# Performance work log

Hardware: AMD Instinct MI355X
Metric: run time of the kernel (lower is better)

## Reference

```python
import jax, jax.numpy as jnp
import numpy as np

N_NODES = 50000
N_EDGES = 800000
IN_F, OUT_F, N_HEADS = 128, 64, 4
NEG_SLOPE = 0.2
EPS = 1e-12


def setup_inputs() -> dict:
    key = jax.random.key(0)
    ks = jax.random.split(key, 6)
    x = jax.random.normal(ks[0], (N_NODES, IN_F), dtype=jnp.float32)
    edge_index = jax.random.randint(ks[1], (2, N_EDGES), 0, N_NODES, dtype=jnp.int32)
    # xavier-uniform-like scaled params
    W = jax.random.normal(ks[2], (IN_F, OUT_F), dtype=jnp.float32) * (2.0 / (IN_F + OUT_F)) ** 0.5
    a_l = jax.random.normal(ks[3], (OUT_F, N_HEADS), dtype=jnp.float32) * (2.0 / (OUT_F + N_HEADS)) ** 0.5
    a_r = jax.random.normal(ks[4], (OUT_F, N_HEADS), dtype=jnp.float32) * (2.0 / (OUT_F + N_HEADS)) ** 0.5
    b = jnp.zeros((OUT_F,), dtype=jnp.float32)
    return {"x": x, "edge_index": edge_index, "W": W, "a_l": a_l, "a_r": a_r, "b": b}


def reference(x, edge_index, W, a_l, a_r, b):
    # GATConv forward (eval mode: attn dropout is identity).
    # Dense NxNxH scatter + L1 normalize in the original == per-row edge softmax
    # over exp(leaky_relu(el[row]+er[col])); honor edge sparsity directly.
    n = x.shape[0]
    h = x @ W                      # [N, D] node representations
    el = h @ a_l                   # [N, H] left (dst/row) scores
    er = h @ a_r                   # [N, H] right (src/col) scores
    row, col = edge_index[0], edge_index[1]
    e = el[row] + er[col]          # [E, H]
    e = jnp.where(e > 0, e, NEG_SLOPE * e)   # leaky_relu(0.2)
    e = jnp.exp(e)
    denom = jax.ops.segment_sum(e, row, num_segments=n)        # [N, H]
    attn = e / jnp.maximum(denom[row], EPS)                    # [E, H] L1-normalized per row
    msg = attn[:, :, None] * h[col][:, None, :]                # [E, H, D]
    out = jax.ops.segment_sum(msg, row, num_segments=n)        # [N, H, D]
    out = out + b                                              # bias broadcast over heads
    return out.reshape(n, -1)                                  # [N, H*D]
```

## Files before the change

kernel.cpp:

```cpp
#include <hip/hip_runtime.h>

#define N_NODES 50000
#define N_EDGES 800000
#define IN_F    128
#define OUT_F   64
#define N_HEADS 4
#define NEG_SLOPE 0.2f
#define EPS 1e-12f

#define NODE_BLOCKS 782
#define NB    391
#define CHUNK 4096
#define NCH   196
#define S2N   (NB * NCH)
#define S2B   75

typedef __attribute__((ext_vector_type(8))) short bf16x8;
typedef __attribute__((ext_vector_type(4))) float f32x4;
typedef __attribute__((ext_vector_type(4))) unsigned int u32x4;

__device__ __forceinline__ unsigned short f2bf(float f) {
    unsigned int u = __float_as_uint(f);
    u += 0x7FFFu + ((u >> 16) & 1u);
    return (unsigned short)(u >> 16);
}
__device__ __forceinline__ float bf_lo(unsigned u) { return __uint_as_float(u << 16); }
__device__ __forceinline__ float bf_hi(unsigned u) { return __uint_as_float(u & 0xFFFF0000u); }

__global__ __launch_bounds__(256) void k_hist_gemm(
    const float* __restrict__ x, const float* __restrict__ W,
    const float* __restrict__ a_l, const float* __restrict__ a_r,
    const int* __restrict__ row, int* __restrict__ histG,
    unsigned short* __restrict__ h_bf,
    float* __restrict__ el, float* __restrict__ er)
{
    __shared__ int hist[NB];
    __shared__ unsigned short xs[64 * 128];
    __shared__ unsigned short wsh[64 * 128];
    const int tid = threadIdx.x;

    if (blockIdx.x < NCH) {
        const int ch = blockIdx.x;
        for (int i = tid; i < NB; i += 256) hist[i] = 0;
        __syncthreads();
        const int e0 = ch * CHUNK + tid * 16;
        #pragma unroll
        for (int q = 0; q < 4; ++q) {
            const int e = e0 + q * 4;
            if (e + 3 < N_EDGES) {
                int4 a = *(const int4*)(row + e);
                atomicAdd(&hist[a.x >> 7], 1); atomicAdd(&hist[a.y >> 7], 1);
                atomicAdd(&hist[a.z >> 7], 1); atomicAdd(&hist[a.w >> 7], 1);
            } else {
                #pragma unroll
                for (int j = 0; j < 4; ++j)
                    if (e + j < N_EDGES) atomicAdd(&hist[row[e + j] >> 7], 1);
            }
        }
        __syncthreads();
        for (int i = tid; i < NB; i += 256) histG[i * NCH + ch] = hist[i];
        return;
    }

    const int node0 = (blockIdx.x - NCH) * 64;

    {
        const int c  = tid & 63;
        const int kq = tid >> 6;
        #pragma unroll
        for (int kb = 0; kb < 32; kb += 8) {
            unsigned pk[4];
            #pragma unroll
            for (int i = 0; i < 4; ++i) {
                const int k = kq * 32 + kb + 2 * i;
                const float v0 = W[k * OUT_F + c];
                const float v1 = W[(k + 1) * OUT_F + c];
                pk[i] = (unsigned)f2bf(v0) | ((unsigned)f2bf(v1) << 16);
            }
            const int cb = (kq * 32 + kb) * 2;
            *(uint4*)((char*)wsh + c * 256 + (cb ^ ((c & 7) << 4))) =
                make_uint4(pk[0], pk[1], pk[2], pk[3]);
        }
    }
    {
        const int r = tid >> 2;
        const int c0 = (tid & 3) * 32;
        const int node = node0 + r;
        unsigned int pk[16];
        if (node < N_NODES) {
            const float* src = x + (size_t)node * IN_F + c0;
            #pragma unroll
            for (int i = 0; i < 8; ++i) {
                float4 v = *(const float4*)(src + 4 * i);
                pk[2 * i + 0] = (unsigned)f2bf(v.x) | ((unsigned)f2bf(v.y) << 16);
                pk[2 * i + 1] = (unsigned)f2bf(v.z) | ((unsigned)f2bf(v.w) << 16);
            }
        } else {
            #pragma unroll
            for (int i = 0; i < 16; ++i) pk[i] = 0;
        }
        #pragma unroll
        for (int q = 0; q < 4; ++q) {
            int cb = c0 * 2 + q * 16;
            *(uint4*)((char*)xs + r * 256 + (cb ^ ((r & 7) << 4))) =
                make_uint4(pk[4 * q], pk[4 * q + 1], pk[4 * q + 2], pk[4 * q + 3]);
        }
    }
    __syncthreads();

    const int w  = tid >> 6, l = tid & 63;
    const int lr = l & 15, lg = l >> 4;
    const int arow = w * 16 + lr;

    bf16x8 afr[4];
    #pragma unroll
    for (int t = 0; t < 4; ++t) {
        int cb = t * 64 + lg * 16;
        afr[t] = *(const bf16x8*)((char*)xs + arow * 256 + (cb ^ ((arow & 7) << 4)));
    }

    const f32x4 zero = {0.f, 0.f, 0.f, 0.f};
    f32x4 acc[4] = {zero, zero, zero, zero};
    #pragma unroll
    for (int nt = 0; nt < 4; ++nt) {
        const int brow = nt * 16 + lr;
        #pragma unroll
        for (int t = 0; t < 4; ++t) {
            int cb = t * 64 + lg * 16;
            bf16x8 bfr = *(const bf16x8*)((char*)wsh + brow * 256 + (cb ^ ((brow & 7) << 4)));
            acc[nt] = __builtin_amdgcn_mfma_f32_16x16x32_bf16(afr[t], bfr, acc[nt], 0, 0, 0);
        }
    }

    #pragma unroll
    for (int r = 0; r < 4; ++r) {
        const int node = node0 + w * 16 + lg * 4 + r;
        if (node < N_NODES) {
            #pragma unroll
            for (int nt = 0; nt < 4; ++nt)
                h_bf[(size_t)node * OUT_F + nt * 16 + lr] = f2bf(acc[nt][r]);
        }
    }

    float4 al4[4], ar4[4];
    #pragma unroll
    for (int nt = 0; nt < 4; ++nt) {
        al4[nt] = *(const float4*)(a_l + (size_t)(nt * 16 + lr) * N_HEADS);
        ar4[nt] = *(const float4*)(a_r + (size_t)(nt * 16 + lr) * N_HEADS);
    }
    #pragma unroll
    for (int r = 0; r < 4; ++r) {
        float4 pl = make_float4(0.f, 0.f, 0.f, 0.f);
        float4 pr = make_float4(0.f, 0.f, 0.f, 0.f);
        #pragma unroll
        for (int nt = 0; nt < 4; ++nt) {
            const float v = acc[nt][r];
            pl.x += v * al4[nt].x; pl.y += v * al4[nt].y;
            pl.z += v * al4[nt].z; pl.w += v * al4[nt].w;
            pr.x += v * ar4[nt].x; pr.y += v * ar4[nt].y;
            pr.z += v * ar4[nt].z; pr.w += v * ar4[nt].w;
        }
        #pragma unroll
        for (int off = 1; off < 16; off <<= 1) {
            pl.x += __shfl_xor(pl.x, off); pl.y += __shfl_xor(pl.y, off);
            pl.z += __shfl_xor(pl.z, off); pl.w += __shfl_xor(pl.w, off);
            pr.x += __shfl_xor(pr.x, off); pr.y += __shfl_xor(pr.y, off);
            pr.z += __shfl_xor(pr.w = pr.w, off) * 0.f + __shfl_xor(pr.z, off);
            pr.w += __shfl_xor(pr.w, off);
        }
        const int node = node0 + w * 16 + lg * 4 + r;
        if (lr == 0 && node < N_NODES) {
            *(float4*)(el + (size_t)node * N_HEADS) = pl;
            *(float4*)(er + (size_t)node * N_HEADS) = pr;
        }
    }
}

__global__ __launch_bounds__(256) void k_scan2_local(
    const int* __restrict__ histG, int* __restrict__ scanHist,
    int* __restrict__ blocksum)
{
    __shared__ int wsum[4];
    const int t = threadIdx.x;
    const int base = blockIdx.x * 1024 + t * 4;

    int4 d = make_int4(0, 0, 0, 0);
    if (base + 3 < S2N) d = *(const int4*)(histG + base);
    else {
        if (base + 0 < S2N) d.x = histG[base + 0];
        if (base + 1 < S2N) d.y = histG[base + 1];
        if (base + 2 < S2N) d.z = histG[base + 2];
        if (base + 3 < S2N) d.w = histG[base + 3];
    }
    const int tsum = d.x + d.y + d.z + d.w;

    const int lane = t & 63, wave = t >> 6;
    int inc = tsum;
    #pragma unroll
    for (int off = 1; off < 64; off <<= 1) {
        int v = __shfl_up(inc, off);
        if (lane >= off) inc += v;
    }
    if (lane == 63) wsum[wave] = inc;
    __syncthreads();

    int woff = 0;
    #pragma unroll
    for (int w = 0; w < 4; ++w) woff += (w < wave) ? wsum[w] : 0;

    const int ex = woff + inc - tsum;
    int4 o;
    o.x = ex; o.y = ex + d.x; o.z = o.y + d.y; o.w = o.z + d.z;
    if (base + 3 < S2N) *(int4*)(scanHist + base) = o;
    else {
        if (base + 0 < S2N) scanHist[base + 0] = o.x;
        if (base + 1 < S2N) scanHist[base + 1] = o.y;
        if (base + 2 < S2N) scanHist[base + 2] = o.z;
        if (base + 3 < S2N) scanHist[base + 3] = o.w;
    }
    if (t == 0) blocksum[blockIdx.x] = wsum[0] + wsum[1] + wsum[2] + wsum[3];
}

__global__ __launch_bounds__(256) void k_scatter(
    const int* __restrict__ row, const int* __restrict__ col,
    const int* __restrict__ scanHist, const int* __restrict__ blocksum,
    unsigned* __restrict__ ebuf)
{
    __shared__ int off[NB];
    __shared__ int bsum[S2B];
    const int ch = blockIdx.x;
    const int t = threadIdx.x;
    if (t < S2B) bsum[t] = blocksum[t];
    __syncthreads();
    if (t == 0) {
        int s = 0;
        for (int i = 0; i < S2B; ++i) { int v = bsum[i]; bsum[i] = s; s += v; }
    }
    __syncthreads();
    for (int i = t; i < NB; i += 256) {
        const int idx = i * NCH + ch;
        off[i] = scanHist[idx] + bsum[idx >> 10];
    }
    __syncthreads();
    const int e0 = ch * CHUNK;
    #pragma unroll
    for (int k = 0; k < 16; ++k) {
        const int e = e0 + t + k * 256;
        if (e < N_EDGES) {
            const int r = row[e], c = col[e];
            const int pos = atomicAdd(&off[r >> 7], 1);
            ebuf[pos] = ((unsigned)(r & 127) << 17) | (unsigned)c;
        }
    }
}

__global__ __launch_bounds__(256) void k_bucket(
    const unsigned* __restrict__ ebuf, const int* __restrict__ scanHist,
    const int* __restrict__ blocksum,
    const float* __restrict__ el, const float* __restrict__ er,
    int* __restrict__ rowptr, uint4* __restrict__ edata)
{
    __shared__ float4 elv[128];
    __shared__ int cnt[128];
    __shared__ int wsum2[2];
    __shared__ int bsum[S2B];
    const int b = blockIdx.x;
    const int t = threadIdx.x;
    const int node0 = b << 7;

    if (t < S2B) bsum[t] = blocksum[t];
    __syncthreads();
    if (t == 0) {
        int s = 0;
        for (int i = 0; i < S2B; ++i) { int v = bsum[i]; bsum[i] = s; s += v; }
    }
    __syncthreads();

    const int i0 = b * NCH;
    const int base = scanHist[i0] + bsum[i0 >> 10];
    int end;
    if (b < NB - 1) {
        const int i1 = (b + 1) * NCH;
        end = scanHist[i1] + bsum[i1 >> 10];
    } else end = N_EDGES;

    if (t < 128) {
        const int node = node0 + t;
        elv[t] = (node < N_NODES) ? *(const float4*)(el + node * 4)
                                  : make_float4(0.f, 0.f, 0.f, 0.f);
        cnt[t] = 0;
    }
    __syncthreads();
    for (int i = base + t; i < end; i += 256)
        atomicAdd(&cnt[ebuf[i] >> 17], 1);
    __syncthreads();

    int inc = 0, val = 0;
    const int lane = t & 63, wave = t >> 6;
    if (t < 128) {
        val = cnt[t];
        inc = val;
        #pragma unroll
        for (int off = 1; off < 64; off <<= 1) {
            int v = __shfl_up(inc, off);
            if (lane >= off) inc += v;
        }
        if (lane == 63) wsum2[wave] = inc;
    }
    __syncthreads();
    int excl = 0;
    if (t < 128) {
        const int woff = (wave == 1) ? wsum2[0] : 0;
        excl = base + woff + inc - val;
        const int node = node0 + t;
        if (node < N_NODES) rowptr[node] = excl;
    }
    if (b == NB - 1 && t == 0) rowptr[N_NODES] = N_EDGES;
    __syncthreads();
    if (t < 128) cnt[t] = excl;
    __syncthreads();

    for (int i = base + t; i < end; i += 256) {
        const unsigned p = ebuf[i];
        const int r = p >> 17;
        const int c = (int)(p & 0x1FFFFu);
        const int pos = atomicAdd(&cnt[r], 1);
        const float4 e4 = elv[r];
        const float4 r4 = *(const float4*)(er + ((unsigned)c << 2));
        float s0 = e4.x + r4.x, s1 = e4.y + r4.y;
        float s2 = e4.z + r4.z, s3 = e4.w + r4.w;
        s0 = s0 > 0.f ? s0 : NEG_SLOPE * s0;
        s1 = s1 > 0.f ? s1 : NEG_SLOPE * s1;
        s2 = s2 > 0.f ? s2 : NEG_SLOPE * s2;
        s3 = s3 > 0.f ? s3 : NEG_SLOPE * s3;
        const unsigned w01 = (unsigned)f2bf(__expf(s0)) | ((unsigned)f2bf(__expf(s1)) << 16);
        const unsigned w23 = (unsigned)f2bf(__expf(s2)) | ((unsigned)f2bf(__expf(s3)) << 16);
        edata[pos] = make_uint4((unsigned)c, w01, w23, 0u);
    }
}

__global__ __launch_bounds__(256) void k_gather(
    const int* __restrict__ rowptr, const u32x4* __restrict__ edata,
    const unsigned short* __restrict__ h_bf, const float* __restrict__ b,
    float* __restrict__ out)
{
    int n = blockIdx.x * 4 + (threadIdx.x >> 6);
    if (n >= N_NODES) return;
    const int lane = threadIdx.x & 63;
    const int g    = lane >> 4;
    const int fq   = lane & 15;

    const int s0 = rowptr[n], s1 = rowptr[n + 1];
    const int nit = (s1 - s0 + 7) >> 3;

    float acc[4][4];
    #pragma unroll
    for (int hd = 0; hd < 4; ++hd)
        #pragma unroll
        for (int f = 0; f < 4; ++f) acc[hd][f] = 0.f;
    float den[4] = {0.f, 0.f, 0.f, 0.f};

    if (nit > 0) {
#define LOADE(ii, E0, E1)                                       \
        {                                                       \
            const int j0 = s0 + (ii) * 8 + 2 * g;               \
            const int j1 = j0 + 1;                              \
            E0 = __builtin_nontemporal_load(&edata[j0 < s1 ? j0 : s1 - 1]); \
            E1 = __builtin_nontemporal_load(&edata[j1 < s1 ? j1 : s1 - 1]); \
            if (j0 >= s1) { E0.y = 0u; E0.z = 0u; }             \
            if (j1 >= s1) { E1.y = 0u; E1.z = 0u; }             \
        }
#define LOADH(E, H)                                                              \
        H = *(const uint2*)(h_bf + (((E.x & 0xFFFFu) << 6) + ((unsigned)fq << 2)));
#define COMP1(E, H)                                                              \
        {                                                                        \
            const float w0 = bf_lo(E.y), w1 = bf_hi(E.y);                        \
            const float w2 = bf_lo(E.z), w3 = bf_hi(E.z);                        \
            const float f0 = bf_lo(H.x), f1 = bf_hi(H.x);                        \
            const float f2 = bf_lo(H.y), f3 = bf_hi(H.y);                        \
            den[0] += w0; den[1] += w1; den[2] += w2; den[3] += w3;              \
            acc[0][0] += w0 * f0; acc[0][1] += w0 * f1;                          \
            acc[0][2] += w0 * f2; acc[0][3] += w0 * f3;                          \
            acc[1][0] += w1 * f0; acc[1][1] += w1 * f1;                          \
            acc[1][2] += w1 * f2; acc[1][3] += w1 * f3;                          \
            acc[2][0] += w2 * f0; acc[2][1] += w2 * f1;                          \
            acc[2][2] += w2 * f2; acc[2][3] += w2 * f3;                          \
            acc[3][0] += w3 * f0; acc[3][1] += w3 * f1;                          \
            acc[3][2] += w3 * f2; acc[3][3] += w3 * f3;                          \
        }

        u32x4 a0, a1, b0, b1;
        uint2 ha0, ha1, hb0, hb1;
        LOADE(0, a0, a1);
        LOADH(a0, ha0); LOADH(a1, ha1);

        for (int it = 0; it < nit; ++it) {
            LOADE(it + 1, b0, b1);
            LOADH(b0, hb0); LOADH(b1, hb1);
            COMP1(a0, ha0);
            COMP1(a1, ha1);
            a0 = b0; a1 = b1; ha0 = hb0; ha1 = hb1;
        }
#undef LOADE
#undef LOADH
#undef COMP1
    }

    #pragma unroll
    for (int hd = 0; hd < 4; ++hd) {
        float v = den[hd];
        v += __shfl_xor(v, 16); v += __shfl_xor(v, 32);
        den[hd] = v;
        #pragma unroll
        for (int f = 0; f < 4; ++f) {
            float u = acc[hd][f];
            u += __shfl_xor(u, 16); u += __shfl_xor(u, 32);
            acc[hd][f] = u;
        }
    }

    const float dg = g == 0 ? den[0] : g == 1 ? den[1] : g == 2 ? den[2] : den[3];
    const float inv = 1.f / fmaxf(dg, EPS);
    f32x4 o;
    o.x = (g == 0 ? acc[0][0] : g == 1 ? acc[1][0] : g == 2 ? acc[2][0] : acc[3][0]);
    o.y = (g == 0 ? acc[0][1] : g == 1 ? acc[1][1] : g == 2 ? acc[2][1] : acc[3][1]);
    o.z = (g == 0 ? acc[0][2] : g == 1 ? acc[1][2] : g == 2 ? acc[2][2] : acc[3][2]);
    o.w = (g == 0 ? acc[0][3] : g == 1 ? acc[1][3] : g == 2 ? acc[2][3] : acc[3][3]);

    const float4 bias = *(const float4*)(b + fq * 4);
    o.x = o.x * inv + bias.x;
    o.y = o.y * inv + bias.y;
    o.z = o.z * inv + bias.z;
    o.w = o.w * inv + bias.w;
    __builtin_nontemporal_store(o,
        (f32x4*)(out + (size_t)n * (N_HEADS * OUT_F) + g * 64 + fq * 4));
}

extern "C" void kernel_launch(void* const* d_in, const int* in_sizes, int n_in,
                              void* d_out, int out_size, void* d_ws, size_t ws_size,
                              hipStream_t stream)
{
    const float* x   = (const float*)d_in[0];
    const int*   ei  = (const int*)d_in[1];
    const float* W   = (const float*)d_in[2];
    const float* a_l = (const float*)d_in[3];
    const float* a_r = (const float*)d_in[4];
    const float* b   = (const float*)d_in[5];
    float* out = (float*)d_out;

    char* ws = (char*)d_ws;
    unsigned short* h_bf = (unsigned short*)(ws);
    float*    el       = (float*)   (ws +  6400000);
    float*    er       = (float*)   (ws +  7200000);
    int*      histG    = (int*)     (ws +  8000000);
    int*      scanHist = (int*)     (ws +  8306544);
    int*      blocksum = (int*)     (ws +  8613088);
    unsigned* ebuf     = (unsigned*)(ws +  8614112);
    int*      rowptr   = (int*)     (ws + 11814112);
    uint4*    edata    = (uint4*)   (ws + 12014128);

    const int* row = ei;
    const int* col = ei + N_EDGES;

    k_hist_gemm  <<<NCH + NODE_BLOCKS, 256, 0, stream>>>(
                     x, W, a_l, a_r, row, histG, h_bf, el, er);
    k_scan2_local<<<S2B, 256, 0, stream>>>(histG, scanHist, blocksum);
    k_scatter    <<<NCH, 256, 0, stream>>>(row, col, scanHist, blocksum, ebuf);
    k_bucket     <<<NB, 256, 0, stream>>>(ebuf, scanHist, blocksum, el, er, rowptr, edata);
    k_gather     <<<N_NODES / 4, 256, 0, stream>>>(rowptr, (const u32x4*)edata, h_bf, b, out);
}
```

Measured before the change: 81.20 us.

## Fuse scan, scatter and bucket kernels into one kernel with grid barriers

Merges the three middle kernels (histogram scan, edge scatter, per-bucket CSR build) into one persistent kernel of 391 blocks. The stages are separated by software grid barriers built on atomic counters, which the first kernel resets. This removes two kernel launches and their inter-kernel gaps. It relies on all 391 blocks being co-resident, which launch_bounds(256,2) is meant to help with, or the barrier deadlocks. The gather kernel also drops its nontemporal loads of the edge data in favour of plain loads.

Measured after the change: 155.5 us. 91.6% more time.

```diff
diff --git a/kernel.cpp b/kernel.cpp
--- a/kernel.cpp
+++ b/kernel.cpp
@@ -17,7 +17,6 @@
 
 typedef __attribute__((ext_vector_type(8))) short bf16x8;
 typedef __attribute__((ext_vector_type(4))) float f32x4;
-typedef __attribute__((ext_vector_type(4))) unsigned int u32x4;
 
 __device__ __forceinline__ unsigned short f2bf(float f) {
     unsigned int u = __float_as_uint(f);
@@ -26,13 +25,26 @@
 }
 __device__ __forceinline__ float bf_lo(unsigned u) { return __uint_as_float(u << 16); }
 __device__ __forceinline__ float bf_hi(unsigned u) { return __uint_as_float(u & 0xFFFF0000u); }
+
+__device__ __forceinline__ void gbar(int* ctr, int nblk) {
+    __syncthreads();
+    if (threadIdx.x == 0) {
+        __threadfence();
+        atomicAdd(ctr, 1);
+        while (__hip_atomic_load(ctr, __ATOMIC_RELAXED, __HIP_MEMORY_SCOPE_AGENT) < nblk)
+            __builtin_amdgcn_s_sleep(1);
+        __threadfence();
+    }
+    __syncthreads();
+}
 
 __global__ __launch_bounds__(256) void k_hist_gemm(
     const float* __restrict__ x, const float* __restrict__ W,
     const float* __restrict__ a_l, const float* __restrict__ a_r,
     const int* __restrict__ row, int* __restrict__ histG,
     unsigned short* __restrict__ h_bf,
-    float* __restrict__ el, float* __restrict__ er)
+    float* __restrict__ el, float* __restrict__ er,
+    int* __restrict__ sync_ctr)
 {
     __shared__ int hist[NB];
     __shared__ unsigned short xs[64 * 128];
@@ -41,6 +53,7 @@
 
     if (blockIdx.x < NCH) {
         const int ch = blockIdx.x;
+        if (ch == 0 && tid < 8) sync_ctr[tid] = 0;
         for (int i = tid; i < NB; i += 256) hist[i] = 0;
         __syncthreads();
         const int e0 = ch * CHUNK + tid * 16;
@@ -165,8 +178,7 @@
             pl.x += __shfl_xor(pl.x, off); pl.y += __shfl_xor(pl.y, off);
             pl.z += __shfl_xor(pl.z, off); pl.w += __shfl_xor(pl.w, off);
             pr.x += __shfl_xor(pr.x, off); pr.y += __shfl_xor(pr.y, off);
-            pr.z += __shfl_xor(pr.w = pr.w, off) * 0.f + __shfl_xor(pr.z, off);
-            pr.w += __shfl_xor(pr.w, off);
+            pr.z += __shfl_xor(pr.z, off); pr.w += __shfl_xor(pr.w, off);
         }
         const int node = node0 + w * 16 + lg * 4 + r;
         if (lr == 0 && node < N_NODES) {
@@ -176,60 +188,60 @@
     }
 }
 
-__global__ __launch_bounds__(256) void k_scan2_local(
+__global__ __launch_bounds__(256, 2) void k_build(
+    const int* __restrict__ row, const int* __restrict__ col,
     const int* __restrict__ histG, int* __restrict__ scanHist,
-    int* __restrict__ blocksum)
-{
-    __shared__ int wsum[4];
-    const int t = threadIdx.x;
-    const int base = blockIdx.x * 1024 + t * 4;
-
-    int4 d = make_int4(0, 0, 0, 0);
-    if (base + 3 < S2N) d = *(const int4*)(histG + base);
-    else {
-        if (base + 0 < S2N) d.x = histG[base + 0];
-        if (base + 1 < S2N) d.y = histG[base + 1];
-        if (base + 2 < S2N) d.z = histG[base + 2];
-        if (base + 3 < S2N) d.w = histG[base + 3];
-    }
-    const int tsum = d.x + d.y + d.z + d.w;
-
-    const int lane = t & 63, wave = t >> 6;
-    int inc = tsum;
-    #pragma unroll
-    for (int off = 1; off < 64; off <<= 1) {
-        int v = __shfl_up(inc, off);
-        if (lane >= off) inc += v;
-    }
-    if (lane == 63) wsum[wave] = inc;
-    __syncthreads();
-
-    int woff = 0;
-    #pragma unroll
-    for (int w = 0; w < 4; ++w) woff += (w < wave) ? wsum[w] : 0;
-
-    const int ex = woff + inc - tsum;
-    int4 o;
-    o.x = ex; o.y = ex + d.x; o.z = o.y + d.y; o.w = o.z + d.z;
-    if (base + 3 < S2N) *(int4*)(scanHist + base) = o;
-    else {
-        if (base + 0 < S2N) scanHist[base + 0] = o.x;
-        if (base + 1 < S2N) scanHist[base + 1] = o.y;
-        if (base + 2 < S2N) scanHist[base + 2] = o.z;
-        if (base + 3 < S2N) scanHist[base + 3] = o.w;
-    }
-    if (t == 0) blocksum[blockIdx.x] = wsum[0] + wsum[1] + wsum[2] + wsum[3];
-}
-
-__global__ __launch_bounds__(256) void k_scatter(
-    const int* __restrict__ row, const int* __restrict__ col,
-    const int* __restrict__ scanHist, const int* __restrict__ blocksum,
-    unsigned* __restrict__ ebuf)
+    int* __restrict__ blocksum,
+    const float* __restrict__ el, const float* __restrict__ er,
+    unsigned* __restrict__ ebuf, int* __restrict__ rowptr,
+    uint4* __restrict__ edata, int* __restrict__ sync_ctr)
 {
     __shared__ int off[NB];
     __shared__ int bsum[S2B];
-    const int ch = blockIdx.x;
+    __shared__ float4 elv[128];
+    __shared__ int cnt[128];
+    __shared__ int wsum4[4];
+    const int blk = blockIdx.x;
     const int t = threadIdx.x;
+
+    if (blk < S2B) {
+        const int base = blk * 1024 + t * 4;
+        int4 d = make_int4(0, 0, 0, 0);
+        if (base + 3 < S2N) d = *(const int4*)(histG + base);
+        else {
+            if (base + 0 < S2N) d.x = histG[base + 0];
+            if (base + 1 < S2N) d.y = histG[base + 1];
+            if (base + 2 < S2N) d.z = histG[base + 2];
+            if (base + 3 < S2N) d.w = histG[base + 3];
+        }
+        const int tsum = d.x + d.y + d.z + d.w;
+        const int lane = t & 63, wave = t >> 6;
+        int inc = tsum;
+        #pragma unroll
+        for (int off2 = 1; off2 < 64; off2 <<= 1) {
+            int v = __shfl_up(inc, off2);
+            if (lane >= off2) inc += v;
+        }
+        if (lane == 63) wsum4[wave] = inc;
+        __syncthreads();
+        int woff = 0;
+        #pragma unroll
+        for (int w = 0; w < 4; ++w) woff += (w < wave) ? wsum4[w] : 0;
+        const int ex = woff + inc - tsum;
+        int4 o;
+        o.x = ex; o.y = ex + d.x; o.z = o.y + d.y; o.w = o.z + d.z;
+        if (base + 3 < S2N) *(int4*)(scanHist + base) = o;
+        else {
+            if (base + 0 < S2N) scanHist[base + 0] = o.x;
+            if (base + 1 < S2N) scanHist[base + 1] = o.y;
+            if (base + 2 < S2N) scanHist[base + 2] = o.z;
+            if (base + 3 < S2N) scanHist[base + 3] = o.w;
+        }
+        if (t == 0) blocksum[blk] = wsum4[0] + wsum4[1] + wsum4[2] + wsum4[3];
+    }
+
+    gbar(&sync_ctr[0], NB);
+
     if (t < S2B) bsum[t] = blocksum[t];
     __syncthreads();
     if (t == 0) {
@@ -237,110 +249,97 @@
         for (int i = 0; i < S2B; ++i) { int v = bsum[i]; bsum[i] = s; s += v; }
     }
     __syncthreads();
-    for (int i = t; i < NB; i += 256) {
-        const int idx = i * NCH + ch;
-        off[i] = scanHist[idx] + bsum[idx >> 10];
-    }
-    __syncthreads();
-    const int e0 = ch * CHUNK;
-    #pragma unroll
-    for (int k = 0; k < 16; ++k) {
-        const int e = e0 + t + k * 256;
-        if (e < N_EDGES) {
-            const int r = row[e], c = col[e];
-            const int pos = atomicAdd(&off[r >> 7], 1);
-            ebuf[pos] = ((unsigned)(r & 127) << 17) | (unsigned)c;
-        }
-    }
-}
-
-__global__ __launch_bounds__(256) void k_bucket(
-    const unsigned* __restrict__ ebuf, const int* __restrict__ scanHist,
-    const int* __restrict__ blocksum,
-    const float* __restrict__ el, const float* __restrict__ er,
-    int* __restrict__ rowptr, uint4* __restrict__ edata)
-{
-    __shared__ float4 elv[128];
-    __shared__ int cnt[128];
-    __shared__ int wsum2[2];
-    __shared__ int bsum[S2B];
-    const int b = blockIdx.x;
-    const int t = threadIdx.x;
-    const int node0 = b << 7;
-
-    if (t < S2B) bsum[t] = blocksum[t];
-    __syncthreads();
-    if (t == 0) {
-        int s = 0;
-        for (int i = 0; i < S2B; ++i) { int v = bsum[i]; bsum[i] = s; s += v; }
-    }
-    __syncthreads();
-
-    const int i0 = b * NCH;
-    const int base = scanHist[i0] + bsum[i0 >> 10];
-    int end;
-    if (b < NB - 1) {
-        const int i1 = (b + 1) * NCH;
-        end = scanHist[i1] + bsum[i1 >> 10];
-    } else end = N_EDGES;
-
-    if (t < 128) {
-        const int node = node0 + t;
-        elv[t] = (node < N_NODES) ? *(const float4*)(el + node * 4)
-                                  : make_float4(0.f, 0.f, 0.f, 0.f);
-        cnt[t] = 0;
-    }
-    __syncthreads();
-    for (int i = base + t; i < end; i += 256)
-        atomicAdd(&cnt[ebuf[i] >> 17], 1);
-    __syncthreads();
-
-    int inc = 0, val = 0;
-    const int lane = t & 63, wave = t >> 6;
-    if (t < 128) {
-        val = cnt[t];
-        inc = val;
-        #pragma unroll
-        for (int off = 1; off < 64; off <<= 1) {
-            int v = __shfl_up(inc, off);
-            if (lane >= off) inc += v;
-        }
-        if (lane == 63) wsum2[wave] = inc;
-    }
-    __syncthreads();
-    int excl = 0;
-    if (t < 128) {
-        const int woff = (wave == 1) ? wsum2[0] : 0;
-        excl = base + woff + inc - val;
-        const int node = node0 + t;
-        if (node < N_NODES) rowptr[node] = excl;
-    }
-    if (b == NB - 1 && t == 0) rowptr[N_NODES] = N_EDGES;
-    __syncthreads();
-    if (t < 128) cnt[t] = excl;
-    __syncthreads();
-
-    for (int i = base + t; i < end; i += 256) {
-        const unsigned p = ebuf[i];
-        const int r = p >> 17;
-        const int c = (int)(p & 0x1FFFFu);
-        const int pos = atomicAdd(&cnt[r], 1);
-        const float4 e4 = elv[r];
-        const float4 r4 = *(const float4*)(er + ((unsigned)c << 2));
-        float s0 = e4.x + r4.x, s1 = e4.y + r4.y;
-        float s2 = e4.z + r4.z, s3 = e4.w + r4.w;
-        s0 = s0 > 0.f ? s0 : NEG_SLOPE * s0;
-        s1 = s1 > 0.f ? s1 : NEG_SLOPE * s1;
-        s2 = s2 > 0.f ? s2 : NEG_SLOPE * s2;
-        s3 = s3 > 0.f ? s3 : NEG_SLOPE * s3;
-        const unsigned w01 = (unsigned)f2bf(__expf(s0)) | ((unsigned)f2bf(__expf(s1)) << 16);
-        const unsigned w23 = (unsigned)f2bf(__expf(s2)) | ((unsigned)f2bf(__expf(s3)) << 16);
-        edata[pos] = make_uint4((unsigned)c, w01, w23, 0u);
+
+    if (blk < NCH) {
+        const int ch = blk;
+        for (int i = t; i < NB; i += 256) {
+            const int idx = i * NCH + ch;
+            off[i] = scanHist[idx] + bsum[idx >> 10];
+        }
+        __syncthreads();
+        const int e0 = ch * CHUNK;
+        #pragma unroll
+        for (int k = 0; k < 16; ++k) {
+            const int e = e0 + t + k * 256;
+            if (e < N_EDGES) {
+                const int r = row[e], c = col[e];
+                const int pos = atomicAdd(&off[r >> 7], 1);
+                ebuf[pos] = ((unsigned)(r & 127) << 17) | (unsigned)c;
+            }
+        }
+    }
+
+    gbar(&sync_ctr[1], NB);
+
+    {
+        const int b = blk;
+        const int node0 = b << 7;
+        const int i0 = b * NCH;
+        const int base = scanHist[i0] + bsum[i0 >> 10];
+        int end;
+        if (b < NB - 1) {
+            const int i1 = (b + 1) * NCH;
+            end = scanHist[i1] + bsum[i1 >> 10];
+        } else end = N_EDGES;
+
+        if (t < 128) {
+            const int node = node0 + t;
+            elv[t] = (node < N_NODES) ? *(const float4*)(el + node * 4)
+                                      : make_float4(0.f, 0.f, 0.f, 0.f);
+            cnt[t] = 0;
+        }
+        __syncthreads();
+        for (int i = base + t; i < end; i += 256)
+            atomicAdd(&cnt[ebuf[i] >> 17], 1);
+        __syncthreads();
+
+        int inc = 0, val = 0;
+        const int lane = t & 63, wave = t >> 6;
+        if (t < 128) {
+            val = cnt[t];
+            inc = val;
+            #pragma unroll
+            for (int off2 = 1; off2 < 64; off2 <<= 1) {
+                int v = __shfl_up(inc, off2);
+                if (lane >= off2) inc += v;
+            }
+            if (lane == 63) wsum4[wave] = inc;
+        }
+        __syncthreads();
+        int excl = 0;
+        if (t < 128) {
+            const int woff = (wave == 1) ? wsum4[0] : 0;
+            excl = base + woff + inc - val;
+            const int node = node0 + t;
+            if (node < N_NODES) rowptr[node] = excl;
+        }
+        if (b == NB - 1 && t == 0) rowptr[N_NODES] = N_EDGES;
+        __syncthreads();
+        if (t < 128) cnt[t] = excl;
+        __syncthreads();
+
+        for (int i = base + t; i < end; i += 256) {
+            const unsigned p = ebuf[i];
+            const int r = p >> 17;
+            const int c = (int)(p & 0x1FFFFu);
+            const int pos = atomicAdd(&cnt[r], 1);
+            const float4 e4 = elv[r];
+            const float4 r4 = *(const float4*)(er + ((unsigned)c << 2));
+            float s0 = e4.x + r4.x, s1 = e4.y + r4.y;
+            float s2 = e4.z + r4.z, s3 = e4.w + r4.w;
+            s0 = s0 > 0.f ? s0 : NEG_SLOPE * s0;
+            s1 = s1 > 0.f ? s1 : NEG_SLOPE * s1;
+            s2 = s2 > 0.f ? s2 : NEG_SLOPE * s2;
+            s3 = s3 > 0.f ? s3 : NEG_SLOPE * s3;
+            const unsigned w01 = (unsigned)f2bf(__expf(s0)) | ((unsigned)f2bf(__expf(s1)) << 16);
+            const unsigned w23 = (unsigned)f2bf(__expf(s2)) | ((unsigned)f2bf(__expf(s3)) << 16);
+            edata[pos] = make_uint4((unsigned)c, w01, w23, 0u);
+        }
     }
 }
 
 __global__ __launch_bounds__(256) void k_gather(
-    const int* __restrict__ rowptr, const u32x4* __restrict__ edata,
+    const int* __restrict__ rowptr, const uint4* __restrict__ edata,
     const unsigned short* __restrict__ h_bf, const float* __restrict__ b,
     float* __restrict__ out)
 {
@@ -361,14 +360,14 @@
     float den[4] = {0.f, 0.f, 0.f, 0.f};
 
     if (nit > 0) {
-#define LOADE(ii, E0, E1)                                       \
-        {                                                       \
-            const int j0 = s0 + (ii) * 8 + 2 * g;               \
-            const int j1 = j0 + 1;                              \
-            E0 = __builtin_nontemporal_load(&edata[j0 < s1 ? j0 : s1 - 1]); \
-            E1 = __builtin_nontemporal_load(&edata[j1 < s1 ? j1 : s1 - 1]); \
-            if (j0 >= s1) { E0.y = 0u; E0.z = 0u; }             \
-            if (j1 >= s1) { E1.y = 0u; E1.z = 0u; }             \
+#define LOADE(ii, E0, E1)                                   \
+        {                                                   \
+            const int j0 = s0 + (ii) * 8 + 2 * g;           \
+            const int j1 = j0 + 1;                          \
+            E0 = edata[j0 < s1 ? j0 : s1 - 1];              \
+            E1 = edata[j1 < s1 ? j1 : s1 - 1];              \
+            if (j0 >= s1) { E0.y = 0u; E0.z = 0u; }         \
+            if (j1 >= s1) { E1.y = 0u; E1.z = 0u; }         \
         }
 #define LOADH(E, H)                                                              \
         H = *(const uint2*)(h_bf + (((E.x & 0xFFFFu) << 6) + ((unsigned)fq << 2)));
@@ -389,7 +388,7 @@
             acc[3][2] += w3 * f2; acc[3][3] += w3 * f3;                          \
         }
 
-        u32x4 a0, a1, b0, b1;
+        uint4 a0, a1, b0, b1;
         uint2 ha0, ha1, hb0, hb1;
         LOADE(0, a0, a1);
         LOADH(a0, ha0); LOADH(a1, ha1);
@@ -458,14 +457,15 @@
     unsigned* ebuf     = (unsigned*)(ws +  8614112);
     int*      rowptr   = (int*)     (ws + 11814112);
     uint4*    edata    = (uint4*)   (ws + 12014128);
+    int*      sync_ctr = (int*)     (ws + 24814144);
 
     const int* row = ei;
     const int* col = ei + N_EDGES;
 
-    k_hist_gemm  <<<NCH + NODE_BLOCKS, 256, 0, stream>>>(
-                     x, W, a_l, a_r, row, histG, h_bf, el, er);
-    k_scan2_local<<<S2B, 256, 0, stream>>>(histG, scanHist, blocksum);
-    k_scatter    <<<NCH, 256, 0, stream>>>(row, col, scanHist, blocksum, ebuf);
-    k_bucket     <<<NB, 256, 0, stream>>>(ebuf, scanHist, blocksum, el, er, rowptr, edata);
-    k_gather     <<<N_NODES / 4, 256, 0, stream>>>(rowptr, (const u32x4*)edata, h_bf, b, out);
-}
+    k_hist_gemm<<<NCH + NODE_BLOCKS, 256, 0, stream>>>(
+                   x, W, a_l, a_r, row, histG, h_bf, el, er, sync_ctr);
+    k_build    <<<NB, 256, 0, stream>>>(
+                   row, col, histG, scanHist, blocksum, el, er,
+                   ebuf, rowptr, edata, sync_ctr);
+    k_gather   <<<N_NODES / 4, 256, 0, stream>>>(rowptr, edata, h_bf, b, out);
+}
```
